# Kernel optimization log

Hardware: AMD Instinct MI355X
Metric: run time of the kernel (lower is better)

The kernel has to match this reference:

```python
import jax, jax.numpy as jnp
import numpy as np

ROT_DIM = 32  # min(32, dim_head)

def rotate_half(t):
    # '... (j d) -> ... j d' with j=2, unbind, cat(-x2, x1)
    x1, x2 = jnp.split(t, 2, axis=-1)
    return jnp.concatenate((-x2, x1), axis=-1)

def apply_rotary(pos, t):
    rot_dim = pos.shape[-1]
    t_rot, t_pass = t[..., :rot_dim], t[..., rot_dim:]
    t_rot = t_rot * jnp.cos(pos) + rotate_half(t_rot) * jnp.sin(pos)
    return jnp.concatenate((t_rot, t_pass), axis=-1)

def setup_inputs() -> dict:
    key = jax.random.key(0)
    k1, k2, k3 = jax.random.split(key, 3)
    b, n, dim = 2, 2048, 2048
    inner = 16 * 128
    x = jax.random.normal(k1, (b, n, dim), dtype=jnp.float32)
    w_qkv = jax.random.normal(k2, (3 * inner, dim), dtype=jnp.float32) * (dim ** -0.5)
    w_out = jax.random.normal(k3, (inner, dim), dtype=jnp.float32) * (inner ** -0.5)
    g = jnp.ones((dim,), dtype=jnp.float32)
    return {"x": x, "w_qkv": w_qkv, "w_out": w_out, "g": g}

def reference(x, w_qkv, w_out, g):
    b, n, dim = x.shape
    h, d = 16, 128
    scale = d ** -0.5
    # NOTE: original code computes qkv from RAW x; the LayerNorm result is unused.
    qkv = jnp.einsum('bnc,fc->bnf', x, w_qkv)  # [b, n, 3*h*d]
    q, k, v = jnp.split(qkv, 3, axis=-1)
    def to_heads(t):  # b n (h d) -> (b h) n d
        return t.reshape(b, n, h, d).transpose(0, 2, 1, 3).reshape(b * h, n, d)
    q, k, v = map(to_heads, (q, k, v))
    # rotary positions: freqs [n, ROT_DIM//2], cat -> [n, ROT_DIM]
    inv_freq = 1.0 / (10000.0 ** (jnp.arange(0, ROT_DIM, 2, dtype=jnp.float32) / ROT_DIM))
    freqs = jnp.arange(n, dtype=jnp.float32)[:, None] * inv_freq[None, :]
    pos = jnp.concatenate((freqs, freqs), axis=-1)  # [n, ROT_DIM]
    q = apply_rotary(pos, q)
    k = apply_rotary(pos, k)
    q = q * scale
    sim = jnp.einsum('bid,bjd->bij', q, k)  # [(b h), n, n]
    causal_mask = jnp.triu(jnp.ones((n, n), dtype=bool), 1)
    neg = -jnp.finfo(sim.dtype).max
    sim = jnp.where(causal_mask[None], neg, sim)
    attn = jax.nn.softmax(sim, axis=-1)
    out = jnp.einsum('bij,bjd->bid', attn, v)  # [(b h), n, d]
    out = out.reshape(b, h, n, d).transpose(0, 2, 1, 3).reshape(b, n, h * d)
    return jnp.einsum('bnf,fc->bnc', out, w_out.T)  # Linear(inner, dim): y = out @ w_out^T with w_out [inner, dim]? see note
```

## Files before the change

### kernel.cpp

```cpp
#include <hip/hip_runtime.h>
#include <hip/hip_bf16.h>
#include <stdint.h>

typedef __bf16 bf16_t;
typedef __bf16 bf16x8 __attribute__((ext_vector_type(8)));
typedef float  f32x4  __attribute__((ext_vector_type(4)));

__device__ __forceinline__ void gload16(const void* gp, void* lp) {
  __builtin_amdgcn_global_load_lds(
      (const __attribute__((address_space(1))) void*)(uintptr_t)gp,
      (__attribute__((address_space(3))) void*)(uintptr_t)lp,
      16, 0, 0);
}

__device__ __forceinline__ f32x4 mfma16(bf16x8 a, bf16x8 b, f32x4 c) {
  return __builtin_amdgcn_mfma_f32_16x16x32_bf16(a, b, c, 0, 0, 0);
}

__device__ __forceinline__ uint32_t pack2(float a, float b) {
  uint16_t ba = __builtin_bit_cast(uint16_t, (bf16_t)a);
  uint16_t bb = __builtin_bit_cast(uint16_t, (bf16_t)b);
  return (uint32_t)ba | ((uint32_t)bb << 16);
}

__global__ __launch_bounds__(256) void cast_f32_to_bf16(const float* __restrict__ in,
                                                        bf16_t* __restrict__ out, int n8) {
  int i = blockIdx.x * 256 + threadIdx.x;
  int stride = gridDim.x * 256;
  for (; i < n8; i += stride) {
    const f32x4* p = (const f32x4*)in + (size_t)i * 2;
    f32x4 a = p[0], b = p[1];
    bf16x8 o;
    o[0] = (bf16_t)a[0]; o[1] = (bf16_t)a[1]; o[2] = (bf16_t)a[2]; o[3] = (bf16_t)a[3];
    o[4] = (bf16_t)b[0]; o[5] = (bf16_t)b[1]; o[6] = (bf16_t)b[2]; o[7] = (bf16_t)b[3];
    ((bf16x8*)out)[i] = o;
  }
}

__global__ __launch_bounds__(512, 2) void gemm_qkv(const bf16_t* __restrict__ A,
                                                   const bf16_t* __restrict__ B,
                                                   bf16_t* __restrict__ C,
                                                   int M, int N, int K) {
  __shared__ __align__(16) bf16_t As[2][256 * 32];
  __shared__ __align__(16) bf16_t Bs[2][384 * 32];
  const int t = threadIdx.x;
  const int wid = t >> 6, l = t & 63;
  const int l15 = l & 15, l4 = l >> 4;
  const int wm = wid >> 2, wn = wid & 3;
  const long m0 = (long)blockIdx.x * 256;
  const long n0 = (long)blockIdx.y * 384;
  const int KT = K >> 5;

  auto stageA = [&](int kt, bf16_t* __restrict__ LB) {
    #pragma unroll
    for (int it = 0; it < 2; ++it) {
      int s = it * 512 + t;
      int r = s >> 2, c = s & 3;
      int cs = c ^ ((r >> 1) & 3);
      gload16(A + (m0 + r) * (long)K + kt * 32 + cs * 8, LB + r * 32 + c * 8);
    }
  };
  auto stageB = [&](int kt, bf16_t* __restrict__ LB) {
    #pragma unroll
    for (int it = 0; it < 3; ++it) {
      int s = it * 512 + t;
      int r = s >> 2, c = s & 3;
      int cs = c ^ ((r >> 1) & 3);
      gload16(B + (n0 + r) * (long)K + kt * 32 + cs * 8, LB + r * 32 + c * 8);
    }
  };
  auto ldfrag = [&](const bf16_t* buf, int rloc) -> bf16x8 {
    int cs = l4 ^ ((rloc >> 1) & 3);
    return *(const bf16x8*)(buf + rloc * 32 + cs * 8);
  };

  f32x4 acc[8][6] = {};

  stageB(0, &Bs[0][0]);
  stageA(0, &As[0][0]);
  stageB(1, &Bs[1][0]);
  asm volatile("s_waitcnt vmcnt(3)" ::: "memory");
  asm volatile("s_barrier" ::: "memory");

  for (int kt = 0; kt < KT; ++kt) {
    const bf16_t* Ab = &As[kt & 1][0];
    const bf16_t* Bb = &Bs[kt & 1][0];
    const bool stA = (kt + 1 < KT), stB = (kt + 2 < KT);

    bf16x8 bfr[6];
    #pragma unroll
    for (int nr = 0; nr < 6; ++nr) bfr[nr] = ldfrag(Bb, wn * 96 + nr * 16 + l15);
    {
      bf16x8 a0 = ldfrag(Ab, wm * 128 + 0 * 16 + l15);
      bf16x8 a1 = ldfrag(Ab, wm * 128 + 1 * 16 + l15);
      bf16x8 a2 = ldfrag(Ab, wm * 128 + 2 * 16 + l15);
      bf16x8 a3 = ldfrag(Ab, wm * 128 + 3 * 16 + l15);
      if (stA) stageA(kt + 1, &As[(kt + 1) & 1][0]);
      asm volatile("s_barrier" ::: "memory");
      __builtin_amdgcn_s_setprio(1);
      #pragma unroll
      for (int nr = 0; nr < 6; ++nr) {
        acc[0][nr] = mfma16(a0, bfr[nr], acc[0][nr]);
        acc[1][nr] = mfma16(a1, bfr[nr], acc[1][nr]);
        acc[2][nr] = mfma16(a2, bfr[nr], acc[2][nr]);
        acc[3][nr] = mfma16(a3, bfr[nr], acc[3][nr]);
      }
      __builtin_amdgcn_s_setprio(0);
      asm volatile("s_barrier" ::: "memory");
    }
    {
      bf16x8 a4 = ldfrag(Ab, wm * 128 + 4 * 16 + l15);
      bf16x8 a5 = ldfrag(Ab, wm * 128 + 5 * 16 + l15);
      bf16x8 a6 = ldfrag(Ab, wm * 128 + 6 * 16 + l15);
      bf16x8 a7 = ldfrag(Ab, wm * 128 + 7 * 16 + l15);
      if (stB) stageB(kt + 2, &Bs[kt & 1][0]);
      asm volatile("s_barrier" ::: "memory");
      __builtin_amdgcn_s_setprio(1);
      #pragma unroll
      for (int nr = 0; nr < 6; ++nr) {
        acc[4][nr] = mfma16(a4, bfr[nr], acc[4][nr]);
        acc[5][nr] = mfma16(a5, bfr[nr], acc[5][nr]);
        acc[6][nr] = mfma16(a6, bfr[nr], acc[6][nr]);
        acc[7][nr] = mfma16(a7, bfr[nr], acc[7][nr]);
      }
      __builtin_amdgcn_s_setprio(0);
      if (stB) asm volatile("s_waitcnt vmcnt(3)" ::: "memory");
      else     asm volatile("s_waitcnt vmcnt(0)" ::: "memory");
      asm volatile("s_barrier" ::: "memory");
    }
  }

  const int nrA = ((128 - ((wn * 96) & 127)) & 127) >> 4;
  const float L2D16 = 0.8304820237218406f;
  const float invf = exp2f(-(float)l15 * L2D16);
  const float qscale = 0.08838834764831845f;
  const float INV2PI = 0.15915494309189535f;
  const float TWOPI  = 6.283185307179586f;
  const bool doRot = (nrA < 6) && ((n0 + wn * 96 + nrA * 16) < 4096);
  #pragma unroll
  for (int mr = 0; mr < 8; ++mr) {
    const long r0 = m0 + wm * 128 + mr * 16 + l4 * 4;
    if (doRot) {
      float sv[4], cv[4];
      #pragma unroll
      for (int i = 0; i < 4; ++i) {
        float ang = (float)((int)(r0 + i) & 2047) * invf;
        float rev = ang * INV2PI;
        rev -= floorf(rev);
        float r2 = rev * TWOPI;
        sv[i] = __sinf(r2);
        cv[i] = __cosf(r2);
      }
      #pragma unroll
      for (int nr = 0; nr < 5; ++nr) {
        if (nr == nrA) {
          #pragma unroll
          for (int i = 0; i < 4; ++i) {
            float a = acc[mr][nr][i], b2 = acc[mr][nr + 1][i];
            acc[mr][nr][i]     = a * cv[i] - b2 * sv[i];
            acc[mr][nr + 1][i] = b2 * cv[i] + a * sv[i];
          }
        }
      }
    }
    #pragma unroll
    for (int nr = 0; nr < 6; ++nr) {
      const long f0 = n0 + wn * 96 + nr * 16;
      if (f0 < 2048) {
        #pragma unroll
        for (int i = 0; i < 4; ++i) acc[mr][nr][i] *= qscale;
      }
      #pragma unroll
      for (int i = 0; i < 4; ++i)
        C[(r0 + i) * N + f0 + l15] = (bf16_t)acc[mr][nr][i];
    }
  }
}

template<bool OUT_BF16>
__global__ __launch_bounds__(512, 2) void gemm8p_bt(const bf16_t* __restrict__ A,
                                                    const bf16_t* __restrict__ B,
                                                    void* __restrict__ Cout,
                                                    int M, int N, int K) {
  __shared__ __align__(16) bf16_t As[2][128 * 64];
  __shared__ __align__(16) bf16_t Bs[2][256 * 64];
  const int t = threadIdx.x;
  const int wid = t >> 6, l = t & 63;
  const int l15 = l & 15, l4 = l >> 4;
  const int wm = wid >> 2, wn = wid & 3;
  const long m0 = (long)blockIdx.x * 128;
  const long n0 = (long)blockIdx.y * 256;
  const int KT = K >> 6;

  auto stageA = [&](int kt, bf16_t* __restrict__ LB) {
    #pragma unroll
    for (int it = 0; it < 2; ++it) {
      int s = it * 512 + t;
      int r = s >> 3, c = s & 7;
      gload16(A + (m0 + r) * (long)K + kt * 64 + ((c ^ (r & 7)) << 3),
              LB + r * 64 + c * 8);
    }
  };
  auto stageB = [&](int kt, bf16_t* __restrict__ LB) {
    #pragma unroll
    for (int it = 0; it < 4; ++it) {
      int s = it * 512 + t;
      int r = s >> 3, c = s & 7;
      gload16(B + (n0 + r) * (long)K + kt * 64 + ((c ^ (r & 7)) << 3),
              LB + r * 64 + c * 8);
    }
  };
  auto ldfrag = [&](const bf16_t* buf, int rloc, int kk) -> bf16x8 {
    return *(const bf16x8*)(buf + rloc * 64 + ((((kk << 2) + l4) ^ (rloc & 7)) << 3));
  };

  f32x4 acc[4][4] = {};

  stageB(0, &Bs[0][0]);
  stageA(0, &As[0][0]);
  stageB(1, &Bs[1][0]);
  asm volatile("s_waitcnt vmcnt(4)" ::: "memory");
  asm volatile("s_barrier" ::: "memory");

  for (int kt = 0; kt < KT; ++kt) {
    const bf16_t* Ab = &As[kt & 1][0];
    const bf16_t* Bb = &Bs[kt & 1][0];
    const bool stA = (kt + 1 < KT), stB = (kt + 2 < KT);

    bf16x8 bfr[4][2];
    #pragma unroll
    for (int nr = 0; nr < 4; ++nr)
      #pragma unroll
      for (int kk = 0; kk < 2; ++kk)
        bfr[nr][kk] = ldfrag(Bb, wn * 64 + nr * 16 + l15, kk);
    {
      bf16x8 a00 = ldfrag(Ab, wm * 64 + 0 * 16 + l15, 0);
      bf16x8 a01 = ldfrag(Ab, wm * 64 + 0 * 16 + l15, 1);
      bf16x8 a10 = ldfrag(Ab, wm * 64 + 1 * 16 + l15, 0);
      bf16x8 a11 = ldfrag(Ab, wm * 64 + 1 * 16 + l15, 1);
      if (stA) stageA(kt + 1, &As[(kt + 1) & 1][0]);
      asm volatile("s_barrier" ::: "memory");
      __builtin_amdgcn_s_setprio(1);
      #pragma unroll
      for (int nr = 0; nr < 4; ++nr) {
        acc[0][nr] = mfma16(a00, bfr[nr][0], acc[0][nr]);
        acc[0][nr] = mfma16(a01, bfr[nr][1], acc[0][nr]);
        acc[1][nr] = mfma16(a10, bfr[nr][0], acc[1][nr]);
        acc[1][nr] = mfma16(a11, bfr[nr][1], acc[1][nr]);
      }
      __builtin_amdgcn_s_setprio(0);
      asm volatile("s_barrier" ::: "memory");
    }
    {
      bf16x8 a00 = ldfrag(Ab, wm * 64 + 2 * 16 + l15, 0);
      bf16x8 a01 = ldfrag(Ab, wm * 64 + 2 * 16 + l15, 1);
      bf16x8 a10 = ldfrag(Ab, wm * 64 + 3 * 16 + l15, 0);
      bf16x8 a11 = ldfrag(Ab, wm * 64 + 3 * 16 + l15, 1);
      if (stB) stageB(kt + 2, &Bs[kt & 1][0]);
      asm volatile("s_barrier" ::: "memory");
      __builtin_amdgcn_s_setprio(1);
      #pragma unroll
      for (int nr = 0; nr < 4; ++nr) {
        acc[2][nr] = mfma16(a00, bfr[nr][0], acc[2][nr]);
        acc[2][nr] = mfma16(a01, bfr[nr][1], acc[2][nr]);
        acc[3][nr] = mfma16(a10, bfr[nr][0], acc[3][nr]);
        acc[3][nr] = mfma16(a11, bfr[nr][1], acc[3][nr]);
      }
      __builtin_amdgcn_s_setprio(0);
      if (stB) asm volatile("s_waitcnt vmcnt(4)" ::: "memory");
      else     asm volatile("s_waitcnt vmcnt(0)" ::: "memory");
      asm volatile("s_barrier" ::: "memory");
    }
  }

  #pragma unroll
  for (int mr = 0; mr < 4; ++mr)
    #pragma unroll
    for (int nr = 0; nr < 4; ++nr)
      #pragma unroll
      for (int i = 0; i < 4; ++i) {
        long r = m0 + wm * 64 + mr * 16 + l4 * 4 + i;
        long c = n0 + wn * 64 + nr * 16 + l15;
        if (OUT_BF16) ((bf16_t*)Cout)[r * N + c] = (bf16_t)acc[mr][nr][i];
        else          ((float*)Cout)[r * N + c] = acc[mr][nr][i];
      }
}

__global__ __launch_bounds__(512, 4) void attn_causal(const bf16_t* __restrict__ qkv,
                                                      bf16_t* __restrict__ ao) {
  const int id = blockIdx.x;
  const int qt = (id < 256) ? (15 - (id >> 5)) : ((id - 256) >> 5);
  const int bh = id & 31;
  const int b = bh >> 4, h = bh & 15;
  const int t = threadIdx.x;
  const int wid = t >> 6, l = t & 63;
  const int l15 = l & 15, l4 = l >> 4;
  __shared__ __align__(16) bf16_t Ks0[64 * 128];
  __shared__ __align__(16) bf16_t Ks1[64 * 128];
  __shared__ __align__(16) bf16_t Vt[2][128 * 64];
  __shared__ __align__(16) bf16_t Pb[8][16 * 64];
  const bf16_t* base = qkv + (long)b * 2048 * 6144 + h * 128;
  const int q0w = qt * 128 + wid * 16;
  bf16x8 qf[4];
  #pragma unroll
  for (int ks = 0; ks < 4; ++ks)
    qf[ks] = *(const bf16x8*)(base + (long)(q0w + l15) * 6144 + ks * 32 + l4 * 8);
  f32x4 o[8] = {};
  float mrun = -1.0e30f, lrun = 0.f;
  bf16_t* pbuf = Pb[wid];
  bf16x8 vr0, vr1;
  const int ntiles = 2 * qt + 2;

  auto stageK = [&](int tile, bf16_t* dst) {
    const bf16_t* src = base + 2048 + (long)tile * 64 * 6144;
    #pragma unroll
    for (int it = 0; it < 2; ++it) {
      int s = it * 512 + t;
      int krow = s >> 4, kc = s & 15;
      int ksc = kc ^ (krow & 7);
      gload16(src + (long)krow * 6144 + ksc * 8, dst + (size_t)s * 8);
    }
  };
  auto loadV = [&](int tile) {
    const bf16_t* vsr = base + 4096 + (long)(tile * 64 + l) * 6144;
    vr0 = *(const bf16x8*)(vsr + wid * 8);
    vr1 = *(const bf16x8*)(vsr + (8 + wid) * 8);
  };
  auto writeVt = [&](bf16_t* vt) {
    #pragma unroll
    for (int it = 0; it < 2; ++it) {
      int c = it * 8 + wid;
      bf16x8 v = it ? vr1 : vr0;
      #pragma unroll
      for (int e = 0; e < 8; ++e) {
        int d = c * 8 + e;
        vt[d * 64 + (((l >> 3) ^ e) * 8) + (l & 7)] = v[e];
      }
    }
  };
  auto compute = [&](int kv0, const bf16_t* ksb, const bf16_t* vt) {
    if (kv0 > q0w + 15) return;
    f32x4 sa[4] = {};
    __builtin_amdgcn_s_setprio(1);
    #pragma unroll
    for (int ks = 0; ks < 4; ++ks) {
      #pragma unroll
      for (int nb = 0; nb < 4; ++nb) {
        int row = nb * 16 + l15;
        int cs = (ks * 4 + l4) ^ (row & 7);
        bf16x8 kf = *(const bf16x8*)(ksb + row * 128 + cs * 8);
        sa[nb] = mfma16(kf, qf[ks], sa[nb]);
      }
    }
    __builtin_amdgcn_s_setprio(0);
    if (kv0 + 63 > q0w) {
      const int q = q0w + l15;
      #pragma unroll
      for (int nb = 0; nb < 4; ++nb)
        #pragma unroll
        for (int i = 0; i < 4; ++i)
          if (kv0 + nb * 16 + l4 * 4 + i > q) sa[nb][i] = -3.0e38f;
    }
    f32x4 mv;
    #pragma unroll
    for (int i = 0; i < 4; ++i)
      mv[i] = fmaxf(fmaxf(sa[0][i], sa[1][i]), fmaxf(sa[2][i], sa[3][i]));
    float pmax = fmaxf(fmaxf(mv[0], mv[1]), fmaxf(mv[2], mv[3]));
    pmax = fmaxf(pmax, __shfl_xor(pmax, 16));
    pmax = fmaxf(pmax, __shfl_xor(pmax, 32));
    if (!__all(pmax - mrun <= 8.0f)) {
      float mnew = fmaxf(mrun, pmax);
      float corr = __expf(mrun - mnew);
      mrun = mnew;
      lrun *= corr;
      float cc[4];
      #pragma unroll
      for (int i = 0; i < 4; ++i) cc[i] = __shfl(corr, l4 * 4 + i);
      #pragma unroll
      for (int nf = 0; nf < 8; ++nf)
        #pragma unroll
        for (int i = 0; i < 4; ++i) o[nf][i] *= cc[i];
    }
    float ps = 0.f;
    #pragma unroll
    for (int nb = 0; nb < 4; ++nb)
      #pragma unroll
      for (int i = 0; i < 4; ++i) {
        float p = __expf(sa[nb][i] - mrun);
        sa[nb][i] = p;
        ps += p;
      }
    ps += __shfl_xor(ps, 16);
    ps += __shfl_xor(ps, 32);
    lrun += ps;
    #pragma unroll
    for (int nb = 0; nb < 4; ++nb) {
      int cw = (nb * 2 + (l4 >> 1)) ^ (l15 & 7);
      uint32_t* dst = (uint32_t*)(pbuf + l15 * 64 + cw * 8 + (l4 & 1) * 4);
      dst[0] = pack2(sa[nb][0], sa[nb][1]);
      dst[1] = pack2(sa[nb][2], sa[nb][3]);
    }
    #pragma unroll
    for (int ks2 = 0; ks2 < 2; ++ks2) {
      bf16x8 pf = *(const bf16x8*)(pbuf + l15 * 64 + (((ks2 * 4 + l4) ^ (l15 & 7)) * 8));
      __builtin_amdgcn_s_setprio(1);
      #pragma unroll
      for (int nf = 0; nf < 8; ++nf) {
        int row = nf * 16 + l15;
        bf16x8 vf = *(const bf16x8*)(vt + row * 64 + (((ks2 * 4 + l4) ^ (row & 7)) * 8));
        o[nf] = mfma16(pf, vf, o[nf]);
      }
      __builtin_amdgcn_s_setprio(0);
    }
  };

  stageK(0, Ks0);
  loadV(0);
  writeVt(Vt[0]);
  __syncthreads();
  for (int tile = 0; tile < ntiles; ++tile) {
    bf16_t* curK = (tile & 1) ? Ks1 : Ks0;
    bf16_t* nxtK = (tile & 1) ? Ks0 : Ks1;
    bf16_t* curV = Vt[tile & 1];
    bf16_t* nxtV = Vt[(tile + 1) & 1];
    const bool pre = (tile + 1 < ntiles);
    if (pre) { stageK(tile + 1, nxtK); loadV(tile + 1); }
    compute(tile * 64, curK, curV);
    if (pre) writeVt(nxtV);
    __syncthreads();
  }
  float linv = 1.f / lrun;
  float li[4];
  #pragma unroll
  for (int i = 0; i < 4; ++i) li[i] = __shfl(linv, l4 * 4 + i);
  bf16_t* aob = ao + (long)b * 2048 * 2048 + h * 128;
  #pragma unroll
  for (int i = 0; i < 4; ++i) {
    long qrow = q0w + l4 * 4 + i;
    #pragma unroll
    for (int nf = 0; nf < 8; ++nf)
      aob[qrow * 2048 + nf * 16 + l15] = (bf16_t)(o[nf][i] * li[i]);
  }
}

extern "C" void kernel_launch(void* const* d_in, const int* in_sizes, int n_in,
                              void* d_out, int out_size, void* d_ws, size_t ws_size,
                              hipStream_t stream) {
  const float* x     = (const float*)d_in[0];
  const float* w_qkv = (const float*)d_in[1];
  const float* w_out = (const float*)d_in[2];
  char* ws = (char*)d_ws;
  bf16_t* xb    = (bf16_t*)(ws + 0L);
  bf16_t* wqkvb = (bf16_t*)(ws + 16777216L);
  bf16_t* woutb = (bf16_t*)(ws + 41943040L);
  bf16_t* qkv   = (bf16_t*)(ws + 50331648L);
  bf16_t* ao    = (bf16_t*)(ws + 100663296L);

  cast_f32_to_bf16<<<2048, 256, 0, stream>>>(x, xb, 1048576);
  cast_f32_to_bf16<<<2048, 256, 0, stream>>>(w_qkv, wqkvb, 1572864);
  cast_f32_to_bf16<<<1024, 256, 0, stream>>>(w_out, woutb, 524288);
  gemm_qkv<<<dim3(16, 16), 512, 0, stream>>>(xb, wqkvb, qkv, 4096, 6144, 2048);
  attn_causal<<<512, 512, 0, stream>>>(qkv, ao);
  gemm8p_bt<false><<<dim3(32, 8), 512, 0, stream>>>(ao, woutb, d_out, 4096, 2048, 2048);
}
```

Before: 223.8 us.

## Shrink QKV GEMM tile to 256x192 and simplify to single-stage prefetch

The QKV projection GEMM block tile shrinks from 256x384 to 256x192, the warp layout changes from 2x4 to 4x2, and the grid doubles to 512 blocks so more CUs get work. The split A/B staggered prefetch with mid-iteration barriers is replaced by a simpler loop that prefetches both A and B for the next k-step and then waits on vmcnt(0) once per iteration. This aims to improve occupancy and wave balance across the device. In exchange it lowers arithmetic intensity per block, adds more global traffic for A, and drops the deeper load/compute overlap of the old schedule.

```diff
diff --git a/kernel.cpp b/kernel.cpp
--- a/kernel.cpp
+++ b/kernel.cpp
@@ -42,13 +42,13 @@
                                                    bf16_t* __restrict__ C,
                                                    int M, int N, int K) {
   __shared__ __align__(16) bf16_t As[2][256 * 32];
-  __shared__ __align__(16) bf16_t Bs[2][384 * 32];
+  __shared__ __align__(16) bf16_t Bs[2][192 * 32];
   const int t = threadIdx.x;
   const int wid = t >> 6, l = t & 63;
   const int l15 = l & 15, l4 = l >> 4;
-  const int wm = wid >> 2, wn = wid & 3;
+  const int wm = wid >> 1, wn = wid & 1;
   const long m0 = (long)blockIdx.x * 256;
-  const long n0 = (long)blockIdx.y * 384;
+  const long n0 = (long)blockIdx.y * 192;
   const int KT = K >> 5;
 
   auto stageA = [&](int kt, bf16_t* __restrict__ LB) {
@@ -62,11 +62,13 @@
   };
   auto stageB = [&](int kt, bf16_t* __restrict__ LB) {
     #pragma unroll
-    for (int it = 0; it < 3; ++it) {
+    for (int it = 0; it < 2; ++it) {
       int s = it * 512 + t;
-      int r = s >> 2, c = s & 3;
-      int cs = c ^ ((r >> 1) & 3);
-      gload16(B + (n0 + r) * (long)K + kt * 32 + cs * 8, LB + r * 32 + c * 8);
+      if (s < 768) {
+        int r = s >> 2, c = s & 3;
+        int cs = c ^ ((r >> 1) & 3);
+        gload16(B + (n0 + r) * (long)K + kt * 32 + cs * 8, LB + r * 32 + c * 8);
+      }
     }
   };
   auto ldfrag = [&](const bf16_t* buf, int rloc) -> bf16x8 {
@@ -74,72 +76,53 @@
     return *(const bf16x8*)(buf + rloc * 32 + cs * 8);
   };
 
-  f32x4 acc[8][6] = {};
-
+  f32x4 acc[4][6] = {};
+
+  stageA(0, &As[0][0]);
   stageB(0, &Bs[0][0]);
-  stageA(0, &As[0][0]);
-  stageB(1, &Bs[1][0]);
-  asm volatile("s_waitcnt vmcnt(3)" ::: "memory");
+  asm volatile("s_waitcnt vmcnt(0)" ::: "memory");
   asm volatile("s_barrier" ::: "memory");
 
   for (int kt = 0; kt < KT; ++kt) {
     const bf16_t* Ab = &As[kt & 1][0];
     const bf16_t* Bb = &Bs[kt & 1][0];
-    const bool stA = (kt + 1 < KT), stB = (kt + 2 < KT);
+    const bool pre = (kt + 1 < KT);
 
     bf16x8 bfr[6];
     #pragma unroll
     for (int nr = 0; nr < 6; ++nr) bfr[nr] = ldfrag(Bb, wn * 96 + nr * 16 + l15);
-    {
-      bf16x8 a0 = ldfrag(Ab, wm * 128 + 0 * 16 + l15);
-      bf16x8 a1 = ldfrag(Ab, wm * 128 + 1 * 16 + l15);
-      bf16x8 a2 = ldfrag(Ab, wm * 128 + 2 * 16 + l15);
-      bf16x8 a3 = ldfrag(Ab, wm * 128 + 3 * 16 + l15);
-      if (stA) stageA(kt + 1, &As[(kt + 1) & 1][0]);
-      asm volatile("s_barrier" ::: "memory");
-      __builtin_amdgcn_s_setprio(1);
-      #pragma unroll
-      for (int nr = 0; nr < 6; ++nr) {
-        acc[0][nr] = mfma16(a0, bfr[nr], acc[0][nr]);
-        acc[1][nr] = mfma16(a1, bfr[nr], acc[1][nr]);
-        acc[2][nr] = mfma16(a2, bfr[nr], acc[2][nr]);
-        acc[3][nr] = mfma16(a3, bfr[nr], acc[3][nr]);
-      }
-      __builtin_amdgcn_s_setprio(0);
-      asm volatile("s_barrier" ::: "memory");
-    }
-    {
-      bf16x8 a4 = ldfrag(Ab, wm * 128 + 4 * 16 + l15);
-      bf16x8 a5 = ldfrag(Ab, wm * 128 + 5 * 16 + l15);
-      bf16x8 a6 = ldfrag(Ab, wm * 128 + 6 * 16 + l15);
-      bf16x8 a7 = ldfrag(Ab, wm * 128 + 7 * 16 + l15);
-      if (stB) stageB(kt + 2, &Bs[kt & 1][0]);
-      asm volatile("s_barrier" ::: "memory");
-      __builtin_amdgcn_s_setprio(1);
-      #pragma unroll
-      for (int nr = 0; nr < 6; ++nr) {
-        acc[4][nr] = mfma16(a4, bfr[nr], acc[4][nr]);
-        acc[5][nr] = mfma16(a5, bfr[nr], acc[5][nr]);
-        acc[6][nr] = mfma16(a6, bfr[nr], acc[6][nr]);
-        acc[7][nr] = mfma16(a7, bfr[nr], acc[7][nr]);
-      }
-      __builtin_amdgcn_s_setprio(0);
-      if (stB) asm volatile("s_waitcnt vmcnt(3)" ::: "memory");
-      else     asm volatile("s_waitcnt vmcnt(0)" ::: "memory");
-      asm volatile("s_barrier" ::: "memory");
-    }
-  }
-
-  const int nrA = ((128 - ((wn * 96) & 127)) & 127) >> 4;
+    bf16x8 a0 = ldfrag(Ab, wm * 64 + 0 * 16 + l15);
+    bf16x8 a1 = ldfrag(Ab, wm * 64 + 1 * 16 + l15);
+    bf16x8 a2 = ldfrag(Ab, wm * 64 + 2 * 16 + l15);
+    bf16x8 a3 = ldfrag(Ab, wm * 64 + 3 * 16 + l15);
+    if (pre) {
+      stageA(kt + 1, &As[(kt + 1) & 1][0]);
+      stageB(kt + 1, &Bs[(kt + 1) & 1][0]);
+    }
+    __builtin_amdgcn_s_setprio(1);
+    #pragma unroll
+    for (int nr = 0; nr < 6; ++nr) {
+      acc[0][nr] = mfma16(a0, bfr[nr], acc[0][nr]);
+      acc[1][nr] = mfma16(a1, bfr[nr], acc[1][nr]);
+      acc[2][nr] = mfma16(a2, bfr[nr], acc[2][nr]);
+      acc[3][nr] = mfma16(a3, bfr[nr], acc[3][nr]);
+    }
+    __builtin_amdgcn_s_setprio(0);
+    asm volatile("s_waitcnt vmcnt(0)" ::: "memory");
+    asm volatile("s_barrier" ::: "memory");
+  }
+
+  const int f0w = (int)(n0 + wn * 96);
+  const int nrA = ((128 - (f0w & 127)) & 127) >> 4;
   const float L2D16 = 0.8304820237218406f;
   const float invf = exp2f(-(float)l15 * L2D16);
   const float qscale = 0.08838834764831845f;
   const float INV2PI = 0.15915494309189535f;
   const float TWOPI  = 6.283185307179586f;
-  const bool doRot = (nrA < 6) && ((n0 + wn * 96 + nrA * 16) < 4096);
+  const bool doRot = (nrA < 6) && (f0w + nrA * 16 < 4096);
   #pragma unroll
-  for (int mr = 0; mr < 8; ++mr) {
-    const long r0 = m0 + wm * 128 + mr * 16 + l4 * 4;
+  for (int mr = 0; mr < 4; ++mr) {
+    const long r0 = m0 + wm * 64 + mr * 16 + l4 * 4;
     if (doRot) {
       float sv[4], cv[4];
       #pragma unroll
@@ -459,7 +442,7 @@
   cast_f32_to_bf16<<<2048, 256, 0, stream>>>(x, xb, 1048576);
   cast_f32_to_bf16<<<2048, 256, 0, stream>>>(w_qkv, wqkvb, 1572864);
   cast_f32_to_bf16<<<1024, 256, 0, stream>>>(w_out, woutb, 524288);
-  gemm_qkv<<<dim3(16, 16), 512, 0, stream>>>(xb, wqkvb, qkv, 4096, 6144, 2048);
+  gemm_qkv<<<dim3(16, 32), 512, 0, stream>>>(xb, wqkvb, qkv, 4096, 6144, 2048);
   attn_causal<<<512, 512, 0, stream>>>(qkv, ao);
   gemm8p_bt<false><<<dim3(32, 8), 512, 0, stream>>>(ao, woutb, d_out, 4096, 2048, 2048);
 }
```

Measured after the change: 238.8 us. 1.07x slower.
